# Optimization experiments

Hardware: AMD Instinct MI355X
Metric: run time of the kernel (lower is better)

## Reference

```python
import jax, jax.numpy as jnp
import numpy as np

N_NODES = 100000
N_EDGES = 1600000
IN_F = 256
OUT_F = 128


def setup_inputs() -> dict:
    key = jax.random.key(0)
    k1, k2, k3, k4, k5, k6 = jax.random.split(key, 6)
    x = jax.random.normal(k1, (N_NODES, IN_F), dtype=jnp.float32)
    edge_src = jax.random.randint(k2, (N_EDGES,), 0, N_NODES, dtype=jnp.int64)
    edge_dst = jax.random.randint(k3, (N_EDGES,), 0, N_NODES, dtype=jnp.int64)
    edge_weight = jax.random.uniform(k4, (N_EDGES,), dtype=jnp.float32)
    stdv = 1.0 / np.sqrt(OUT_F)
    w = jax.random.uniform(k5, (IN_F, OUT_F), dtype=jnp.float32, minval=-stdv, maxval=stdv)
    b = jax.random.uniform(k6, (OUT_F,), dtype=jnp.float32, minval=-stdv, maxval=stdv)
    return {"x": x, "edge_src": edge_src, "edge_dst": edge_dst,
            "edge_weight": edge_weight, "w": w, "b": b}


def reference(x, edge_src, edge_dst, edge_weight, w, b):
    # dense feature transform: [N, in] @ [in, out] -> [N, out]
    h = x @ w
    # sparse adjacency SpMM: out[i] = sum_{e: dst[e]==i} a[e] * h[src[e]]
    msgs = h[edge_src] * edge_weight[:, None]          # [E, out]
    agg = jax.ops.segment_sum(msgs, edge_dst, num_segments=N_NODES)
    return agg + b
```

## Files before the change

### kernel.cpp

```cpp
#include <hip/hip_runtime.h>

#define N_NODES 100000
#define N_EDGES 1600000
#define IN_F 256
#define OUT_F 128

#define NBUCK 1563
#define NCH   250
#define CH    6400
#define BCAP  2048
#define SCAP  256
#define HALF  782

typedef __attribute__((ext_vector_type(8))) short bf16x8;
typedef __attribute__((ext_vector_type(4))) float f32x4;

static __device__ __forceinline__ unsigned f2bf_u(float f) {
    unsigned u = __float_as_uint(f);
    return (u + 0x7FFFu + ((u >> 16) & 1u)) >> 16;
}
static __device__ __forceinline__ float bf2f(short s) {
    return __uint_as_float(((unsigned)(unsigned short)s) << 16);
}
static __device__ __forceinline__ bf16x8 pack_bf16x8(float4 a, float4 b) {
    union { unsigned u[4]; bf16x8 v; } r;
    r.u[0] = f2bf_u(a.x) | (f2bf_u(a.y) << 16);
    r.u[1] = f2bf_u(a.z) | (f2bf_u(a.w) << 16);
    r.u[2] = f2bf_u(b.x) | (f2bf_u(b.y) << 16);
    r.u[3] = f2bf_u(b.z) | (f2bf_u(b.w) << 16);
    return r.v;
}

__global__ __launch_bounds__(1024) void init_kernel(int* __restrict__ gadd,
                                                    const float* __restrict__ w,
                                                    unsigned short* __restrict__ wtf) {
    const int t = threadIdx.x;
    if (blockIdx.x == 0) {
        for (int i = t; i < 8 * NBUCK; i += 1024) gadd[i] = 0;
        return;
    }
    const int id = (blockIdx.x - 1) * 1024 + t;
    const int f = id >> 6, lane = id & 63;
    const int ks = f >> 3, nt = f & 7;
    const int m = lane & 15, q = lane >> 4;
    const int row = nt * 16 + m;
    const int col0 = ks * 32 + q * 8;
    unsigned short* o = wtf + (size_t)f * 512 + lane * 8;
    #pragma unroll
    for (int j = 0; j < 8; ++j)
        o[j] = (unsigned short)f2bf_u(w[(size_t)(col0 + j) * OUT_F + row]);
}

__global__ __launch_bounds__(1024) void part_kernel(const int* __restrict__ edge_src,
                                                    const int* __restrict__ edge_dst,
                                                    const float* __restrict__ edge_weight,
                                                    int* __restrict__ gadd,
                                                    int2* __restrict__ part) {
    __shared__ int h[NBUCK];
    const int t = threadIdx.x;
    const int c = blockIdx.x;
    const int stripe = c & 7;
    const int sbase = stripe << 8;
    for (int i = t; i < NBUCK; i += 1024) h[i] = 0;
    __syncthreads();

    const int e0 = c * CH;
    const int4*   d4 = (const int4*)(edge_dst + e0);
    const int4*   s4 = (const int4*)(edge_src + e0);
    const float4* w4 = (const float4*)(edge_weight + e0);

    int4   dd[2];
    int4   ss[2];
    float4 ww[2];
    bool   val[2];
    #pragma unroll
    for (int i = 0; i < 2; ++i) {
        const int k = t + i * 1024;
        val[i] = (k < CH / 4);
        if (val[i]) {
            dd[i] = d4[k];
            ss[i] = s4[k];
            ww[i] = w4[k];
            atomicAdd(&h[dd[i].x >> 6], 1);
            atomicAdd(&h[dd[i].y >> 6], 1);
            atomicAdd(&h[dd[i].z >> 6], 1);
            atomicAdd(&h[dd[i].w >> 6], 1);
        }
    }
    __syncthreads();

    int* g = gadd + stripe * NBUCK;
    for (int i = t; i < NBUCK; i += 1024) {
        const int cnt = h[i];
        int base = 0;
        if (cnt > 0) base = atomicAdd(&g[i], cnt);
        h[i] = (i << 11) + sbase + base;
    }
    __syncthreads();

    #pragma unroll
    for (int i = 0; i < 2; ++i) {
        if (val[i]) {
            int b, pos;
            b = dd[i].x >> 6; pos = atomicAdd(&h[b], 1);
            if (pos < (b << 11) + sbase + SCAP)
                part[pos] = make_int2(ss[i].x | ((dd[i].x & 63) << 24), __float_as_int(ww[i].x));
            b = dd[i].y >> 6; pos = atomicAdd(&h[b], 1);
            if (pos < (b << 11) + sbase + SCAP)
                part[pos] = make_int2(ss[i].y | ((dd[i].y & 63) << 24), __float_as_int(ww[i].y));
            b = dd[i].z >> 6; pos = atomicAdd(&h[b], 1);
            if (pos < (b << 11) + sbase + SCAP)
                part[pos] = make_int2(ss[i].z | ((dd[i].z & 63) << 24), __float_as_int(ww[i].z));
            b = dd[i].w >> 6; pos = atomicAdd(&h[b], 1);
            if (pos < (b << 11) + sbase + SCAP)
                part[pos] = make_int2(ss[i].w | ((dd[i].w & 63) << 24), __float_as_int(ww[i].w));
        }
    }
}

__global__ __launch_bounds__(256) void gemm_mfma_kernel(const float* __restrict__ x,
                                                        const unsigned short* __restrict__ wtf,
                                                        unsigned short* __restrict__ hb) {
    const int t = threadIdx.x;
    const int wave = t >> 6, lane = t & 63;
    const int m = lane & 15, quad = lane >> 4;
    const int row0 = blockIdx.x * 128 + wave * 32;

    int rA = row0 + m;      if (rA >= N_NODES) rA = N_NODES - 1;
    int rB = row0 + 16 + m; if (rB >= N_NODES) rB = N_NODES - 1;
    const float4* xA = (const float4*)(x + (size_t)rA * IN_F) + quad * 2;
    const float4* xB = (const float4*)(x + (size_t)rB * IN_F) + quad * 2;

    f32x4 acc[2][8];
    #pragma unroll
    for (int tl = 0; tl < 2; ++tl)
        #pragma unroll
        for (int nt = 0; nt < 8; ++nt) acc[tl][nt] = (f32x4){0.f, 0.f, 0.f, 0.f};

    const bf16x8* wf = (const bf16x8*)wtf;
    #pragma unroll
    for (int ks = 0; ks < 8; ++ks) {
        const bf16x8 a0 = pack_bf16x8(xA[ks * 8], xA[ks * 8 + 1]);
        const bf16x8 a1 = pack_bf16x8(xB[ks * 8], xB[ks * 8 + 1]);
        #pragma unroll
        for (int nt = 0; nt < 8; ++nt) {
            const bf16x8 bf = wf[(size_t)(ks * 8 + nt) * 64 + lane];
            acc[0][nt] = __builtin_amdgcn_mfma_f32_16x16x32_bf16(a0, bf, acc[0][nt], 0, 0, 0);
            acc[1][nt] = __builtin_amdgcn_mfma_f32_16x16x32_bf16(a1, bf, acc[1][nt], 0, 0, 0);
        }
    }

    #pragma unroll
    for (int tl = 0; tl < 2; ++tl) {
        const int tile_base = row0 + tl * 16;
        #pragma unroll
        for (int nt = 0; nt < 8; ++nt) {
            #pragma unroll
            for (int r = 0; r < 4; ++r) {
                const int orow = tile_base + quad * 4 + r;
                if (orow < N_NODES)
                    hb[(size_t)orow * OUT_F + nt * 16 + m] = (unsigned short)f2bf_u(acc[tl][nt][r]);
            }
        }
    }
}

static __device__ __forceinline__ void spmm_body(const int bucket,
                                                 const unsigned short* __restrict__ hb,
                                                 const int* __restrict__ gadd,
                                                 const int2* __restrict__ part,
                                                 const float* __restrict__ b,
                                                 float* __restrict__ out) {
    __shared__ int lh[64];
    __shared__ int lstart[65];
    __shared__ int lcur[64];
    __shared__ int cs[8];
    __shared__ int csum[9];
    __shared__ int2 list[BCAP];

    const int t = threadIdx.x;
    const int base = bucket * 64;

    if (t < 64) lh[t] = 0;
    if (t < 8) {
        int cc = gadd[t * NBUCK + bucket];
        cs[t] = cc > SCAP ? SCAP : cc;
    }
    __syncthreads();
    if (t == 0) {
        int a = 0;
        csum[0] = 0;
        #pragma unroll
        for (int i = 0; i < 8; ++i) { a += cs[i]; csum[i + 1] = a; }
    }
    __syncthreads();
    const int total = csum[8];

    int2 stash[4];
    int  sn[4];
    #pragma unroll
    for (int sub = 0; sub < 4; ++sub) {
        const int idx = sub * 512 + t;
        sn[sub] = -1;
        if (idx < total) {
            int sdx = 0;
            #pragma unroll
            for (int q = 1; q < 8; ++q) sdx += (idx >= csum[q]);
            const int local = idx - csum[sdx];
            const int2 en = part[((size_t)bucket << 11) + (sdx << 8) + local];
            const int n = ((unsigned)en.x) >> 24;
            sn[sub] = n;
            stash[sub] = make_int2(en.x & 0xFFFFFF, en.y);
            atomicAdd(&lh[n], 1);
        }
    }
    __syncthreads();

    if (t < 64) {
        const int v = lh[t];
        int s = v;
        #pragma unroll
        for (int off = 1; off < 64; off <<= 1) {
            const int o = __shfl_up(s, off);
            if (t >= off) s += o;
        }
        lstart[t] = s - v;
        lcur[t]   = s - v;
        if (t == 63) lstart[64] = s;
    }
    __syncthreads();

    #pragma unroll
    for (int sub = 0; sub < 4; ++sub) {
        if (sn[sub] >= 0) {
            const int pos = atomicAdd(&lcur[sn[sub]], 1);
            list[pos] = stash[sub];
        }
    }
    __syncthreads();

    const int j = t & 15;
    const float4* b4 = (const float4*)b;
    const float4 bb0 = b4[j * 2];
    const float4 bb1 = b4[j * 2 + 1];

    #pragma unroll
    for (int g = 0; g < 2; ++g) {
        const int n = g * 32 + (t >> 4);
        const int node = base + n;
        if (node >= N_NODES) continue;
        float4 acc0 = bb0, acc1 = bb1;
        int p = lstart[n];
        const int p1 = lstart[n + 1];
        for (; p + 4 <= p1; p += 4) {
            const int2 sw0 = list[p];
            const int2 sw1 = list[p + 1];
            const int2 sw2 = list[p + 2];
            const int2 sw3 = list[p + 3];
            const bf16x8 h0 = *(const bf16x8*)(hb + (size_t)sw0.x * OUT_F + j * 8);
            const bf16x8 h1 = *(const bf16x8*)(hb + (size_t)sw1.x * OUT_F + j * 8);
            const bf16x8 h2 = *(const bf16x8*)(hb + (size_t)sw2.x * OUT_F + j * 8);
            const bf16x8 h3 = *(const bf16x8*)(hb + (size_t)sw3.x * OUT_F + j * 8);
            const float w0 = __int_as_float(sw0.y);
            const float w1 = __int_as_float(sw1.y);
            const float w2 = __int_as_float(sw2.y);
            const float w3 = __int_as_float(sw3.y);
            acc0.x += w0 * bf2f(h0[0]); acc0.y += w0 * bf2f(h0[1]);
            acc0.z += w0 * bf2f(h0[2]); acc0.w += w0 * bf2f(h0[3]);
            acc1.x += w0 * bf2f(h0[4]); acc1.y += w0 * bf2f(h0[5]);
            acc1.z += w0 * bf2f(h0[6]); acc1.w += w0 * bf2f(h0[7]);
            acc0.x += w1 * bf2f(h1[0]); acc0.y += w1 * bf2f(h1[1]);
            acc0.z += w1 * bf2f(h1[2]); acc0.w += w1 * bf2f(h1[3]);
            acc1.x += w1 * bf2f(h1[4]); acc1.y += w1 * bf2f(h1[5]);
            acc1.z += w1 * bf2f(h1[6]); acc1.w += w1 * bf2f(h1[7]);
            acc0.x += w2 * bf2f(h2[0]); acc0.y += w2 * bf2f(h2[1]);
            acc0.z += w2 * bf2f(h2[2]); acc0.w += w2 * bf2f(h2[3]);
            acc1.x += w2 * bf2f(h2[4]); acc1.y += w2 * bf2f(h2[5]);
            acc1.z += w2 * bf2f(h2[6]); acc1.w += w2 * bf2f(h2[7]);
            acc0.x += w3 * bf2f(h3[0]); acc0.y += w3 * bf2f(h3[1]);
            acc0.z += w3 * bf2f(h3[2]); acc0.w += w3 * bf2f(h3[3]);
            acc1.x += w3 * bf2f(h3[4]); acc1.y += w3 * bf2f(h3[5]);
            acc1.z += w3 * bf2f(h3[6]); acc1.w += w3 * bf2f(h3[7]);
        }
        for (; p < p1; ++p) {
            const int2 sw = list[p];
            const float wgt = __int_as_float(sw.y);
            const bf16x8 hv = *(const bf16x8*)(hb + (size_t)sw.x * OUT_F + j * 8);
            acc0.x += wgt * bf2f(hv[0]); acc0.y += wgt * bf2f(hv[1]);
            acc0.z += wgt * bf2f(hv[2]); acc0.w += wgt * bf2f(hv[3]);
            acc1.x += wgt * bf2f(hv[4]); acc1.y += wgt * bf2f(hv[5]);
            acc1.z += wgt * bf2f(hv[6]); acc1.w += wgt * bf2f(hv[7]);
        }
        float4* o4 = (float4*)(out + (size_t)node * OUT_F + j * 8);
        o4[0] = acc0;
        o4[1] = acc1;
    }
}

__global__ __launch_bounds__(512) void spmm_a_kernel(const unsigned short* __restrict__ hb,
                                                     const int* __restrict__ gadd,
                                                     const int2* __restrict__ part,
                                                     const float* __restrict__ b,
                                                     float* __restrict__ out) {
    spmm_body(blockIdx.x, hb, gadd, part, b, out);
}
__global__ __launch_bounds__(512) void spmm_b_kernel(const unsigned short* __restrict__ hb,
                                                     const int* __restrict__ gadd,
                                                     const int2* __restrict__ part,
                                                     const float* __restrict__ b,
                                                     float* __restrict__ out) {
    spmm_body(blockIdx.x + HALF, hb, gadd, part, b, out);
}

extern "C" void kernel_launch(void* const* d_in, const int* in_sizes, int n_in,
                              void* d_out, int out_size, void* d_ws, size_t ws_size,
                              hipStream_t stream) {
    const float* x           = (const float*)d_in[0];
    const int*   edge_src    = (const int*)d_in[1];
    const int*   edge_dst    = (const int*)d_in[2];
    const float* edge_weight = (const float*)d_in[3];
    const float* w           = (const float*)d_in[4];
    const float* b           = (const float*)d_in[5];
    float* out = (float*)d_out;

    char* ws = (char*)d_ws;
    size_t off = 0;
    unsigned short* hb  = (unsigned short*)(ws + off);
    off += (size_t)N_NODES * OUT_F * 2;           off = (off + 15) & ~(size_t)15;
    unsigned short* wtf = (unsigned short*)(ws + off);
    off += (size_t)IN_F * OUT_F * 2;              off = (off + 15) & ~(size_t)15;
    int* gadd = (int*)(ws + off);
    off += (size_t)8 * NBUCK * 4;                 off = (off + 15) & ~(size_t)15;
    int2* part = (int2*)(ws + off);
    off += (size_t)NBUCK * BCAP * 8;

    init_kernel<<<5, 1024, 0, stream>>>(gadd, w, wtf);
    part_kernel<<<NCH, 1024, 0, stream>>>(edge_src, edge_dst, edge_weight, gadd, part);
    gemm_mfma_kernel<<<(N_NODES + 127) / 128, 256, 0, stream>>>(x, wtf, hb);
    spmm_a_kernel<<<HALF, 512, 0, stream>>>(hb, gadd, part, b, out);
    spmm_b_kernel<<<NBUCK - HALF, 512, 0, stream>>>(hb, gadd, part, b, out);
}
```

Baseline: 288.8 us.

## Stage GEMM weight fragments in LDS and use 8 waves of 16 rows

The GEMM kernel now copies the whole bf16 weight fragment array (64 KB) into shared memory once per block and reads B fragments from LDS instead of global memory. Blocks grow to 512 threads, with each wave computing one 16-row tile instead of two, so more waves are available to hide latency. The cost is a 64 KB shared allocation that limits how many blocks fit per CU, a block-wide sync, and less B-fragment reuse in registers per wave.

```diff
diff --git a/kernel.cpp b/kernel.cpp
--- a/kernel.cpp
+++ b/kernel.cpp
@@ -118,49 +118,49 @@
     }
 }
 
-__global__ __launch_bounds__(256) void gemm_mfma_kernel(const float* __restrict__ x,
+__global__ __launch_bounds__(512) void gemm_mfma_kernel(const float* __restrict__ x,
                                                         const unsigned short* __restrict__ wtf,
                                                         unsigned short* __restrict__ hb) {
+    __shared__ unsigned short bs[64 * 512];
     const int t = threadIdx.x;
+
+    {
+        const uint4* wsrc = (const uint4*)wtf;
+        uint4* wdst = (uint4*)bs;
+        #pragma unroll
+        for (int i = 0; i < 8; ++i) wdst[t + i * 512] = wsrc[t + i * 512];
+    }
+    __syncthreads();
+
     const int wave = t >> 6, lane = t & 63;
     const int m = lane & 15, quad = lane >> 4;
-    const int row0 = blockIdx.x * 128 + wave * 32;
-
-    int rA = row0 + m;      if (rA >= N_NODES) rA = N_NODES - 1;
-    int rB = row0 + 16 + m; if (rB >= N_NODES) rB = N_NODES - 1;
-    const float4* xA = (const float4*)(x + (size_t)rA * IN_F) + quad * 2;
-    const float4* xB = (const float4*)(x + (size_t)rB * IN_F) + quad * 2;
-
-    f32x4 acc[2][8];
-    #pragma unroll
-    for (int tl = 0; tl < 2; ++tl)
-        #pragma unroll
-        for (int nt = 0; nt < 8; ++nt) acc[tl][nt] = (f32x4){0.f, 0.f, 0.f, 0.f};
-
-    const bf16x8* wf = (const bf16x8*)wtf;
+    const int row0 = blockIdx.x * 128 + wave * 16;
+
+    int r = row0 + m; if (r >= N_NODES) r = N_NODES - 1;
+    const float4* xr = (const float4*)(x + (size_t)r * IN_F) + quad * 2;
+
+    f32x4 acc[8];
+    #pragma unroll
+    for (int nt = 0; nt < 8; ++nt) acc[nt] = (f32x4){0.f, 0.f, 0.f, 0.f};
+
+    const bf16x8* bfrag = (const bf16x8*)bs;
     #pragma unroll
     for (int ks = 0; ks < 8; ++ks) {
-        const bf16x8 a0 = pack_bf16x8(xA[ks * 8], xA[ks * 8 + 1]);
-        const bf16x8 a1 = pack_bf16x8(xB[ks * 8], xB[ks * 8 + 1]);
+        const bf16x8 a = pack_bf16x8(xr[ks * 8], xr[ks * 8 + 1]);
         #pragma unroll
         for (int nt = 0; nt < 8; ++nt) {
-            const bf16x8 bf = wf[(size_t)(ks * 8 + nt) * 64 + lane];
-            acc[0][nt] = __builtin_amdgcn_mfma_f32_16x16x32_bf16(a0, bf, acc[0][nt], 0, 0, 0);
-            acc[1][nt] = __builtin_amdgcn_mfma_f32_16x16x32_bf16(a1, bf, acc[1][nt], 0, 0, 0);
-        }
-    }
-
-    #pragma unroll
-    for (int tl = 0; tl < 2; ++tl) {
-        const int tile_base = row0 + tl * 16;
-        #pragma unroll
-        for (int nt = 0; nt < 8; ++nt) {
-            #pragma unroll
-            for (int r = 0; r < 4; ++r) {
-                const int orow = tile_base + quad * 4 + r;
-                if (orow < N_NODES)
-                    hb[(size_t)orow * OUT_F + nt * 16 + m] = (unsigned short)f2bf_u(acc[tl][nt][r]);
-            }
+            const bf16x8 bf = bfrag[(ks * 8 + nt) * 64 + lane];
+            acc[nt] = __builtin_amdgcn_mfma_f32_16x16x32_bf16(a, bf, acc[nt], 0, 0, 0);
+        }
+    }
+
+    #pragma unroll
+    for (int nt = 0; nt < 8; ++nt) {
+        #pragma unroll
+        for (int rr = 0; rr < 4; ++rr) {
+            const int orow = row0 + quad * 4 + rr;
+            if (orow < N_NODES)
+                hb[(size_t)orow * OUT_F + nt * 16 + m] = (unsigned short)f2bf_u(acc[nt][rr]);
         }
     }
 }
@@ -336,7 +336,7 @@
 
     init_kernel<<<5, 1024, 0, stream>>>(gadd, w, wtf);
     part_kernel<<<NCH, 1024, 0, stream>>>(edge_src, edge_dst, edge_weight, gadd, part);
-    gemm_mfma_kernel<<<(N_NODES + 127) / 128, 256, 0, stream>>>(x, wtf, hb);
+    gemm_mfma_kernel<<<(N_NODES + 127) / 128, 512, 0, stream>>>(x, wtf, hb);
     spmm_a_kernel<<<HALF, 512, 0, stream>>>(hb, gadd, part, b, out);
     spmm_b_kernel<<<NBUCK - HALF, 512, 0, stream>>>(hb, gadd, part, b, out);
 }
```

Result: faster. 279.2 us (-3.3%).
